# Kernel optimization log

Hardware: AMD Instinct MI355X
Metric: run time of the kernel (lower is better)

The kernel has to match this reference:

```python
import jax, jax.numpy as jnp
import numpy as np

NUM_NODES = 100000
NUM_REL_P1 = 238  # num_relations + 1 (extra column for self-connection relation id -1)
B = 32768
S = 16
D_IN = 256
D_OUT = 256


def setup_inputs() -> dict:
    key = jax.random.key(0)
    k1, k2, k3, k4, k5 = jax.random.split(key, 5)
    neighbors = jax.random.randint(k1, (B, S), 0, NUM_NODES)          # sampled neighbor node ids
    relations = jax.random.randint(k2, (B, S), 0, NUM_REL_P1)          # sampled relation ids
    features = jax.random.normal(k3, (NUM_NODES, D_IN), dtype=jnp.float32)
    weight = jax.random.normal(k4, (D_OUT, D_IN), dtype=jnp.float32) * (1.0 / np.sqrt(D_IN))
    relation_weight = jax.random.normal(k5, (D_OUT, NUM_REL_P1), dtype=jnp.float32) * 0.05
    return {"neighbors": neighbors, "relations": relations, "features": features,
            "weight": weight, "relation_weight": relation_weight}


def reference(neighbors, relations, features, weight, relation_weight):
    # gather sampled neighbor embeddings: [B, S, D_in]
    neighbor_emb = features[neighbors]
    # mean-aggregate over the sample dim: [B, D_in]
    agg_neighbors = neighbor_emb.mean(axis=1)
    # linear transform: [B, D_in] @ [D_in, D_out] -> [B, D_out]
    agg_neighbors = agg_neighbors @ weight.T
    # gather + mean relation embeddings: [B, S, D_out] -> [B, D_out]
    agg_relations = relation_weight.T[relations].mean(axis=1)
    return jax.nn.relu(agg_neighbors + agg_relations)
```

## Files before the change

kernel.cpp:

```cpp
#include <hip/hip_runtime.h>

#define B_ROWS 32768
#define S_SAMP 16
#define NRELS  238
#define DIM    256

typedef __attribute__((ext_vector_type(8))) short  short8;
typedef __attribute__((ext_vector_type(4))) float  f32x4;

static __device__ __forceinline__ unsigned short f2bf(float f) {
    unsigned int u = __float_as_uint(f);
    u += 0x7FFFu + ((u >> 16) & 1u);
    return (unsigned short)(u >> 16);
}
static __device__ __forceinline__ float bf2f(unsigned short u) {
    return __uint_as_float(((unsigned int)u) << 16);
}

__global__ __launch_bounds__(256) void prep_kernel(const float* __restrict__ W,
                                                   const float* __restrict__ RW,
                                                   unsigned short* __restrict__ Wb,
                                                   float* __restrict__ RWT) {
    int i = blockIdx.x * 256 + threadIdx.x;
    if (i < DIM * DIM) Wb[i] = f2bf(W[i]);
    if (i < NRELS * DIM) {
        int r = i >> 8;
        int d = i & 255;
        RWT[i] = RW[d * NRELS + r];
    }
}

__global__ __launch_bounds__(256) void gather_kernel(const int* __restrict__ nbr,
                                                     const int* __restrict__ rels,
                                                     const float* __restrict__ feat,
                                                     const float* __restrict__ RWT,
                                                     unsigned short* __restrict__ A,
                                                     unsigned short* __restrict__ RelA) {
    const int lane = threadIdx.x & 63;
    const int row  = __builtin_amdgcn_readfirstlane(blockIdx.x * 4 + (threadIdx.x >> 6));
    const int* nb = nbr  + row * S_SAMP;
    const int* rl = rels + row * S_SAMP;

    float a0 = 0.f, a1 = 0.f, a2 = 0.f, a3 = 0.f;
    float r0 = 0.f, r1 = 0.f, r2 = 0.f, r3 = 0.f;
#pragma unroll
    for (int s = 0; s < S_SAMP; ++s) {
        const int nid = nb[s];
        const int rid = rl[s];
        const float4 f = *(const float4*)(feat + (size_t)nid * DIM + lane * 4);
        const float4 g = *(const float4*)(RWT + rid * DIM + lane * 4);
        a0 += f.x; a1 += f.y; a2 += f.z; a3 += f.w;
        r0 += g.x; r1 += g.y; r2 += g.z; r3 += g.w;
    }
    const float sc = 1.0f / 16.0f;
    ushort4 pa, pr;
    pa.x = f2bf(a0 * sc); pa.y = f2bf(a1 * sc); pa.z = f2bf(a2 * sc); pa.w = f2bf(a3 * sc);
    pr.x = f2bf(r0 * sc); pr.y = f2bf(r1 * sc); pr.z = f2bf(r2 * sc); pr.w = f2bf(r3 * sc);
    *(ushort4*)(A    + (size_t)row * DIM + lane * 4) = pa;
    *(ushort4*)(RelA + (size_t)row * DIM + lane * 4) = pr;
}

__global__ __launch_bounds__(256) void gemm_kernel(const unsigned short* __restrict__ A,
                                                   const unsigned short* __restrict__ Wb,
                                                   const unsigned short* __restrict__ RelA,
                                                   float* __restrict__ out) {
    __shared__ unsigned short Abuf[64][264];
    const int tid  = threadIdx.x;
    const int lane = tid & 63;
    const int wid  = tid >> 6;
    const int m0   = blockIdx.x * 64;

#pragma unroll
    for (int j = 0; j < 8; ++j) {
        int idx = (j * 256 + tid) * 8;
        int r = idx >> 8;
        int c = idx & 255;
        uint4 v = *(const uint4*)(A + (size_t)m0 * DIM + idx);
        *(uint4*)&Abuf[r][c] = v;
    }
    __syncthreads();

    const int mrow = wid * 16 + (lane & 15);
    const int quad = lane >> 4;

    f32x4 acc[16];
#pragma unroll
    for (int n = 0; n < 16; ++n) acc[n] = (f32x4){0.f, 0.f, 0.f, 0.f};

#pragma unroll
    for (int kk = 0; kk < 8; ++kk) {
        short8 af = *(const short8*)&Abuf[mrow][kk * 32 + quad * 8];
#pragma unroll
        for (int n = 0; n < 16; ++n) {
            short8 bf = *(const short8*)(Wb + (size_t)(n * 16 + (lane & 15)) * DIM
                                            + kk * 32 + quad * 8);
            acc[n] = __builtin_amdgcn_mfma_f32_16x16x32_bf16(af, bf, acc[n], 0, 0, 0);
        }
    }

    const int col0  = lane & 15;
    const int rbase = m0 + wid * 16 + quad * 4;
#pragma unroll
    for (int n = 0; n < 16; ++n) {
        const int col = n * 16 + col0;
#pragma unroll
        for (int i = 0; i < 4; ++i) {
            const int r = rbase + i;
            float v = acc[n][i] + bf2f(RelA[(size_t)r * DIM + col]);
            out[(size_t)r * DIM + col] = v > 0.f ? v : 0.f;
        }
    }
}

extern "C" void kernel_launch(void* const* d_in, const int* in_sizes, int n_in,
                              void* d_out, int out_size, void* d_ws, size_t ws_size,
                              hipStream_t stream) {
    const int*   neighbors = (const int*)d_in[0];
    const int*   relations = (const int*)d_in[1];
    const float* features  = (const float*)d_in[2];
    const float* weight    = (const float*)d_in[3];
    const float* relw      = (const float*)d_in[4];
    float* out = (float*)d_out;

    char* ws = (char*)d_ws;
    unsigned short* Wb   = (unsigned short*)ws;
    float*          RWT  = (float*)(ws + 131072);
    unsigned short* A    = (unsigned short*)(ws + 131072 + 243712);
    unsigned short* RelA = (unsigned short*)(ws + 131072 + 243712 + 16777216);

    prep_kernel<<<256, 256, 0, stream>>>(weight, relw, Wb, RWT);
    gather_kernel<<<B_ROWS / 4, 256, 0, stream>>>(neighbors, relations, features, RWT, A, RelA);
    gemm_kernel<<<B_ROWS / 64, 256, 0, stream>>>(A, Wb, RelA, out);
}
```

Baseline: 265.2 us.

## Transform all node features before gathering, then aggregate bf16 projected rows

Uses linearity of the mean to reorder the work: every node feature row is first multiplied by the weight with MFMA into a bf16 table, and the aggregate kernel then gathers and averages projected rows plus bf16 relation rows and applies ReLU. The gather now reads 512-byte bf16 rows instead of 1 KB fp32 rows, and the intermediate A/RelA buffers disappear. In exchange the GEMM grows from 32768 to 100000 rows and all features are streamed once. Rounding to bf16 before averaging also changes numerics slightly.

Result: slower. 320.8 us (+21.0%).

```diff
diff --git a/kernel.cpp b/kernel.cpp
--- a/kernel.cpp
+++ b/kernel.cpp
@@ -1,9 +1,10 @@
 #include <hip/hip_runtime.h>
 
-#define B_ROWS 32768
-#define S_SAMP 16
-#define NRELS  238
-#define DIM    256
+#define B_ROWS  32768
+#define S_SAMP  16
+#define NRELS   238
+#define DIM     256
+#define N_NODES 100000
 
 typedef __attribute__((ext_vector_type(8))) short  short8;
 typedef __attribute__((ext_vector_type(4))) float  f32x4;
@@ -14,56 +15,25 @@
     return (unsigned short)(u >> 16);
 }
 static __device__ __forceinline__ float bf2f(unsigned short u) {
-    return __uint_as_float(((unsigned int)u) << 16);
+    return __uint_as_float(((unsigned int)u) << 32 - 16);
 }
 
 __global__ __launch_bounds__(256) void prep_kernel(const float* __restrict__ W,
                                                    const float* __restrict__ RW,
                                                    unsigned short* __restrict__ Wb,
-                                                   float* __restrict__ RWT) {
+                                                   unsigned short* __restrict__ RWTb) {
     int i = blockIdx.x * 256 + threadIdx.x;
     if (i < DIM * DIM) Wb[i] = f2bf(W[i]);
     if (i < NRELS * DIM) {
         int r = i >> 8;
         int d = i & 255;
-        RWT[i] = RW[d * NRELS + r];
+        RWTb[i] = f2bf(RW[d * NRELS + r]);
     }
 }
 
-__global__ __launch_bounds__(256) void gather_kernel(const int* __restrict__ nbr,
-                                                     const int* __restrict__ rels,
-                                                     const float* __restrict__ feat,
-                                                     const float* __restrict__ RWT,
-                                                     unsigned short* __restrict__ A,
-                                                     unsigned short* __restrict__ RelA) {
-    const int lane = threadIdx.x & 63;
-    const int row  = __builtin_amdgcn_readfirstlane(blockIdx.x * 4 + (threadIdx.x >> 6));
-    const int* nb = nbr  + row * S_SAMP;
-    const int* rl = rels + row * S_SAMP;
-
-    float a0 = 0.f, a1 = 0.f, a2 = 0.f, a3 = 0.f;
-    float r0 = 0.f, r1 = 0.f, r2 = 0.f, r3 = 0.f;
-#pragma unroll
-    for (int s = 0; s < S_SAMP; ++s) {
-        const int nid = nb[s];
-        const int rid = rl[s];
-        const float4 f = *(const float4*)(feat + (size_t)nid * DIM + lane * 4);
-        const float4 g = *(const float4*)(RWT + rid * DIM + lane * 4);
-        a0 += f.x; a1 += f.y; a2 += f.z; a3 += f.w;
-        r0 += g.x; r1 += g.y; r2 += g.z; r3 += g.w;
-    }
-    const float sc = 1.0f / 16.0f;
-    ushort4 pa, pr;
-    pa.x = f2bf(a0 * sc); pa.y = f2bf(a1 * sc); pa.z = f2bf(a2 * sc); pa.w = f2bf(a3 * sc);
-    pr.x = f2bf(r0 * sc); pr.y = f2bf(r1 * sc); pr.z = f2bf(r2 * sc); pr.w = f2bf(r3 * sc);
-    *(ushort4*)(A    + (size_t)row * DIM + lane * 4) = pa;
-    *(ushort4*)(RelA + (size_t)row * DIM + lane * 4) = pr;
-}
-
-__global__ __launch_bounds__(256) void gemm_kernel(const unsigned short* __restrict__ A,
-                                                   const unsigned short* __restrict__ Wb,
-                                                   const unsigned short* __restrict__ RelA,
-                                                   float* __restrict__ out) {
+__global__ __launch_bounds__(256) void transform_kernel(const float* __restrict__ F,
+                                                        const unsigned short* __restrict__ Wb,
+                                                        unsigned short* __restrict__ FT) {
     __shared__ unsigned short Abuf[64][264];
     const int tid  = threadIdx.x;
     const int lane = tid & 63;
@@ -71,12 +41,16 @@
     const int m0   = blockIdx.x * 64;
 
 #pragma unroll
-    for (int j = 0; j < 8; ++j) {
-        int idx = (j * 256 + tid) * 8;
-        int r = idx >> 8;
-        int c = idx & 255;
-        uint4 v = *(const uint4*)(A + (size_t)m0 * DIM + idx);
-        *(uint4*)&Abuf[r][c] = v;
+    for (int j = 0; j < 16; ++j) {
+        int fid = j * 256 + tid;
+        int r  = fid >> 6;
+        int c4 = fid & 63;
+        int gr = m0 + r;
+        if (gr >= N_NODES) gr = N_NODES - 1;
+        float4 v = *(const float4*)(F + (size_t)gr * DIM + c4 * 4);
+        ushort4 p;
+        p.x = f2bf(v.x); p.y = f2bf(v.y); p.z = f2bf(v.z); p.w = f2bf(v.w);
+        *(ushort4*)&Abuf[r][c4 * 4] = p;
     }
     __syncthreads();
 
@@ -106,10 +80,40 @@
 #pragma unroll
         for (int i = 0; i < 4; ++i) {
             const int r = rbase + i;
-            float v = acc[n][i] + bf2f(RelA[(size_t)r * DIM + col]);
-            out[(size_t)r * DIM + col] = v > 0.f ? v : 0.f;
+            if (r < N_NODES) FT[(size_t)r * DIM + col] = f2bf(acc[n][i]);
         }
     }
+}
+
+__global__ __launch_bounds__(256) void aggregate_kernel(const int* __restrict__ nbr,
+                                                        const int* __restrict__ rels,
+                                                        const unsigned short* __restrict__ FT,
+                                                        const unsigned short* __restrict__ RWTb,
+                                                        float* __restrict__ out) {
+    const int lane = threadIdx.x & 63;
+    const int row  = __builtin_amdgcn_readfirstlane(blockIdx.x * 4 + (threadIdx.x >> 6));
+    const int* nb = nbr  + row * S_SAMP;
+    const int* rl = rels + row * S_SAMP;
+
+    float a0 = 0.f, a1 = 0.f, a2 = 0.f, a3 = 0.f;
+#pragma unroll
+    for (int s = 0; s < S_SAMP; ++s) {
+        const int nid = nb[s];
+        const int rid = rl[s];
+        const ushort4 f = *(const ushort4*)(FT   + (size_t)nid * DIM + lane * 4);
+        const ushort4 g = *(const ushort4*)(RWTb + (size_t)rid * DIM + lane * 4);
+        a0 += bf2f(f.x) + bf2f(g.x);
+        a1 += bf2f(f.y) + bf2f(g.y);
+        a2 += bf2f(f.z) + bf2f(g.z);
+        a3 += bf2f(f.w) + bf2f(g.w);
+    }
+    const float sc = 1.0f / 16.0f;
+    float4 o;
+    o.x = fmaxf(a0 * sc, 0.f);
+    o.y = fmaxf(a1 * sc, 0.f);
+    o.z = fmaxf(a2 * sc, 0.f);
+    o.w = fmaxf(a3 * sc, 0.f);
+    *(float4*)(out + (size_t)row * DIM + lane * 4) = o;
 }
 
 extern "C" void kernel_launch(void* const* d_in, const int* in_sizes, int n_in,
@@ -124,11 +128,10 @@
 
     char* ws = (char*)d_ws;
     unsigned short* Wb   = (unsigned short*)ws;
-    float*          RWT  = (float*)(ws + 131072);
-    unsigned short* A    = (unsigned short*)(ws + 131072 + 243712);
-    unsigned short* RelA = (unsigned short*)(ws + 131072 + 243712 + 16777216);
+    unsigned short* RWTb = (unsigned short*)(ws + 131072);
+    unsigned short* FT   = (unsigned short*)(ws + 253952);
 
-    prep_kernel<<<256, 256, 0, stream>>>(weight, relw, Wb, RWT);
-    gather_kernel<<<B_ROWS / 4, 256, 0, stream>>>(neighbors, relations, features, RWT, A, RelA);
-    gemm_kernel<<<B_ROWS / 64, 256, 0, stream>>>(A, Wb, RelA, out);
+    prep_kernel<<<256, 256, 0, stream>>>(weight, relw, Wb, RWTb);
+    transform_kernel<<<(N_NODES + 63) / 64, 256, 0, stream>>>(features, Wb, FT);
+    aggregate_kernel<<<B_ROWS / 4, 256, 0, stream>>>(neighbors, relations, FT, RWTb, out);
 }
```
